# Kernel optimization log

Hardware: AMD Instinct MI355X
Metric: run time of the kernel (lower is better)

Reference implementation:

```python
import jax, jax.numpy as jnp
import numpy as np

ITEM_NUM = 1_000_000
MAXLEN = 200
H = 128
NH = 2
NB = 2
B = 2048
FLOAT_MIN = -1000.0
EPS = 1e-8


def _ln(x, g, b):
    mu = jnp.mean(x, axis=-1, keepdims=True)
    var = jnp.mean((x - mu) ** 2, axis=-1, keepdims=True)
    return (x - mu) / jnp.sqrt(var + EPS) * g + b


def setup_inputs() -> dict:
    key = jax.random.key(0)
    ks = jax.random.split(key, 32)
    s = 1.0 / np.sqrt(H)
    d = {}
    d['user_ids'] = jax.random.randint(ks[0], (B,), 0, 100000)
    d['log_seqs'] = jax.random.randint(ks[1], (B, MAXLEN), 0, ITEM_NUM)
    d['pos_seqs'] = jax.random.randint(ks[2], (B, MAXLEN), 0, ITEM_NUM)
    d['neg_seqs'] = jax.random.randint(ks[3], (B, MAXLEN), 0, ITEM_NUM)
    item = jax.random.normal(ks[4], (ITEM_NUM + 1, H), jnp.float32) * 0.02
    d['item_table'] = item.at[0].set(0.0)  # padding_idx=0
    pos = jax.random.normal(ks[5], (MAXLEN + 1, H), jnp.float32) * 0.02
    d['pos_table'] = pos.at[0].set(0.0)
    # per-block stacked params, torch Linear layout [out,in]
    d['qw'] = jax.random.normal(ks[6], (NB, H, H), jnp.float32) * s
    d['kw'] = jax.random.normal(ks[7], (NB, H, H), jnp.float32) * s
    d['vw'] = jax.random.normal(ks[8], (NB, H, H), jnp.float32) * s
    d['ow'] = jax.random.normal(ks[9], (NB, H, H), jnp.float32) * s
    d['qb'] = jnp.zeros((NB, H), jnp.float32)
    d['kb'] = jnp.zeros((NB, H), jnp.float32)
    d['vb'] = jnp.zeros((NB, H), jnp.float32)
    d['ob'] = jnp.zeros((NB, H), jnp.float32)
    d['w1'] = jax.random.normal(ks[10], (NB, H, H), jnp.float32) * s  # conv1 k=1 == linear
    d['b1'] = jnp.zeros((NB, H), jnp.float32)
    d['w2'] = jax.random.normal(ks[11], (NB, H, H), jnp.float32) * s
    d['b2'] = jnp.zeros((NB, H), jnp.float32)
    d['ln1_g'] = jnp.ones((NB, H), jnp.float32)
    d['ln1_b'] = jnp.zeros((NB, H), jnp.float32)
    d['ln2_g'] = jnp.ones((NB, H), jnp.float32)
    d['ln2_b'] = jnp.zeros((NB, H), jnp.float32)
    d['lnf_g'] = jnp.ones((H,), jnp.float32)
    d['lnf_b'] = jnp.zeros((H,), jnp.float32)
    return d


def reference(item_table, pos_table, qw, qb, kw, kb, vw, vb, ow, ob,
              ln1_g, ln1_b, w1, b1, w2, b2, ln2_g, ln2_b, lnf_g, lnf_b,
              user_ids, log_seqs, pos_seqs, neg_seqs):
    Bb, L = log_seqs.shape
    hd = H // NH
    seqs = item_table[log_seqs] * jnp.asarray(np.sqrt(H), jnp.float32)  # [B,L,H]
    poss = jnp.arange(1, L + 1)[None, :] * (log_seqs != 0)
    seqs = seqs + pos_table[poss]
    causal = jnp.triu(jnp.ones((L, L), bool), k=1)  # True = masked (future)
    for i in range(NB):
        x = seqs
        Q = (x @ qw[i].T + qb[i]).reshape(Bb, L, NH, hd).transpose(0, 2, 1, 3)
        K = (x @ kw[i].T + kb[i]).reshape(Bb, L, NH, hd).transpose(0, 2, 1, 3)
        V = (x @ vw[i].T + vb[i]).reshape(Bb, L, NH, hd).transpose(0, 2, 1, 3)
        scores = jnp.einsum('bhqd,bhkd->bhqk', Q, K) / jnp.asarray(np.sqrt(hd), jnp.float32)
        scores = jnp.where(causal, FLOAT_MIN, scores)
        attn_w = jax.nn.softmax(scores, axis=-1)
        attn = jnp.einsum('bhqk,bhkd->bhqd', attn_w, V)
        attn = attn.transpose(0, 2, 1, 3).reshape(Bb, L, H)
        mha = attn @ ow[i].T + ob[i]
        seqs = _ln(x + mha, ln1_g[i], ln1_b[i])
        ff = jax.nn.relu(seqs @ w1[i].T + b1[i]) @ w2[i].T + b2[i]
        seqs = _ln(seqs + ff, ln2_g[i], ln2_b[i])
    log_feats = _ln(seqs, lnf_g, lnf_b)
    pos_logits = jnp.sum(log_feats * item_table[pos_seqs], axis=-1)
    neg_logits = jnp.sum(log_feats * item_table[neg_seqs], axis=-1)
    return (pos_logits, neg_logits)
```

## Files before the change

### kernel.cpp

```cpp
#include <hip/hip_runtime.h>
#include <math.h>

#define L 200
#define H 128
#define HD 64
#define NB 2
#define BTOT 2048
#define HH (H * H)
#define MTOT (BTOT * L)
#define XSS 136

typedef short bf16x8 __attribute__((ext_vector_type(8)));
typedef float f32x4 __attribute__((ext_vector_type(4)));
typedef unsigned short u16;

#define MFMA16 __builtin_amdgcn_mfma_f32_16x16x32_bf16

__device__ __forceinline__ u16 f2bf(float f) {
    unsigned u = __builtin_bit_cast(unsigned, f);
    u = u + 0x7fffu + ((u >> 16) & 1u);
    return (u16)(u >> 16);
}
__device__ __forceinline__ float bf2f(u16 s) {
    return __builtin_bit_cast(float, ((unsigned)s) << 16);
}
__device__ __forceinline__ bf16x8 pack8(float4 a, float4 b, float sc) {
    bf16x8 r;
    r[0] = (short)f2bf(a.x * sc); r[1] = (short)f2bf(a.y * sc);
    r[2] = (short)f2bf(a.z * sc); r[3] = (short)f2bf(a.w * sc);
    r[4] = (short)f2bf(b.x * sc); r[5] = (short)f2bf(b.y * sc);
    r[6] = (short)f2bf(b.z * sc); r[7] = (short)f2bf(b.w * sc);
    return r;
}

__global__ __launch_bounds__(256) void cvt_kernel(const float* __restrict__ src,
                                                  u16* __restrict__ dst, int n8) {
    int i = blockIdx.x * 256 + threadIdx.x;
    if (i >= n8) return;
    float4 a0 = ((const float4*)src)[i * 2];
    float4 a1 = ((const float4*)src)[i * 2 + 1];
    ((bf16x8*)dst)[i] = pack8(a0, a1, 1.0f);
}

__global__ __launch_bounds__(256) void embed_kernel(const int* __restrict__ ids,
                                                    const float4* __restrict__ item,
                                                    const float4* __restrict__ post,
                                                    u16* __restrict__ X, int M) {
    int idx = blockIdx.x * 256 + threadIdx.x;
    if (idx >= M * 16) return;
    int r = idx >> 4, c8 = idx & 15;
    int id = ids[r];
    int l = r % L;
    int p = (id != 0) ? (l + 1) : 0;
    float4 a0 = item[(size_t)id * 32 + c8 * 2];
    float4 a1 = item[(size_t)id * 32 + c8 * 2 + 1];
    float4 p0 = post[(size_t)p * 32 + c8 * 2];
    float4 p1 = post[(size_t)p * 32 + c8 * 2 + 1];
    const float sc = 11.313708498984761f;
    float4 o0 = make_float4(a0.x * sc + p0.x, a0.y * sc + p0.y, a0.z * sc + p0.z, a0.w * sc + p0.w);
    float4 o1 = make_float4(a1.x * sc + p1.x, a1.y * sc + p1.y, a1.z * sc + p1.z, a1.w * sc + p1.w);
    *(bf16x8*)&X[(size_t)r * 128 + c8 * 8] = pack8(o0, o1, 1.0f);
}

__global__ __launch_bounds__(256) void qkv_kernel(const u16* __restrict__ X,
        const u16* __restrict__ wq, const u16* __restrict__ wk, const u16* __restrict__ wv,
        const float* __restrict__ qb, const float* __restrict__ kb, const float* __restrict__ vb,
        u16* __restrict__ Qo, u16* __restrict__ Ko, u16* __restrict__ Vo, int M) {
    __shared__ u16 Xs[128 * XSS];
    __shared__ u16 Ot[4][16 * XSS];
    int tid = threadIdx.x, w = tid >> 6, lane = tid & 63, g = lane >> 4, l15 = lane & 15;
    int row0 = blockIdx.x * 128;
#pragma unroll
    for (int it = 0; it < 8; ++it) {
        int idx = it * 256 + tid;
        int r = idx >> 4, c8 = idx & 15;
        size_t gr = (size_t)min(row0 + r, M - 1);
        *(bf16x8*)&Xs[r * XSS + c8 * 8] = *(const bf16x8*)(X + gr * 128 + c8 * 8);
    }
    __syncthreads();

    int arow = w * 32 + l15;
    int ko = g * 8;

#pragma unroll
    for (int p = 0; p < 3; ++p) {
        const u16* Wp = p == 0 ? wq : (p == 1 ? wk : wv);
        const float* bp = p == 0 ? qb : (p == 1 ? kb : vb);
        u16* Op = p == 0 ? Qo : (p == 1 ? Ko : Vo);
        const float scale = p == 0 ? 0.125f : 1.0f;

        f32x4 acc[2][8];
#pragma unroll
        for (int nt = 0; nt < 8; ++nt) {
            float bv = bp[nt * 16 + l15];
            acc[0][nt] = (f32x4){bv, bv, bv, bv};
            acc[1][nt] = (f32x4){bv, bv, bv, bv};
        }
#pragma unroll
        for (int kc = 0; kc < 4; ++kc) {
            bf16x8 a0 = *(const bf16x8*)&Xs[arow * XSS + kc * 32 + ko];
            bf16x8 a1 = *(const bf16x8*)&Xs[(arow + 16) * XSS + kc * 32 + ko];
#pragma unroll
            for (int nt = 0; nt < 8; ++nt) {
                bf16x8 b = *(const bf16x8*)(Wp + ((size_t)(nt * 16 + l15) << 7) + kc * 32 + ko);
                acc[0][nt] = MFMA16(a0, b, acc[0][nt], 0, 0, 0);
                acc[1][nt] = MFMA16(a1, b, acc[1][nt], 0, 0, 0);
            }
        }
#pragma unroll
        for (int mt = 0; mt < 2; ++mt) {
#pragma unroll
            for (int r = 0; r < 4; ++r) {
                int ml = g * 4 + r;
#pragma unroll
                for (int nt = 0; nt < 8; ++nt)
                    Ot[w][ml * XSS + nt * 16 + l15] = f2bf(acc[mt][nt][r] * scale);
            }
            asm volatile("s_waitcnt lgkmcnt(0)" ::: "memory");
#pragma unroll
            for (int j = 0; j < 4; ++j) {
                int chunk = j * 64 + lane;
                int rr = chunk >> 4, c16 = chunk & 15;
                bf16x8 v = *(const bf16x8*)&Ot[w][rr * XSS + c16 * 8];
                int grow = row0 + w * 32 + mt * 16 + rr;
                if (grow < M) *(bf16x8*)(Op + (size_t)grow * 128 + c16 * 8) = v;
            }
            asm volatile("s_waitcnt lgkmcnt(0)" ::: "memory");
        }
    }
}

__global__ __launch_bounds__(256) void oproj_ffn1_kernel(const u16* __restrict__ A,
        const u16* __restrict__ Wo, const float* __restrict__ ob,
        const u16* __restrict__ Xres, const float* __restrict__ gma, const float* __restrict__ bta,
        const u16* __restrict__ W1, const float* __restrict__ b1f,
        u16* __restrict__ Xout, u16* __restrict__ F1, int M) {
    __shared__ u16 Xs[128 * XSS];
    __shared__ u16 Ot[4][16 * XSS];
    int tid = threadIdx.x, w = tid >> 6, lane = tid & 63, g = lane >> 4, l15 = lane & 15;
    int row0 = blockIdx.x * 128;
    int rw = row0 + w * 32;
    size_t ar0 = (size_t)min(rw + l15, M - 1) * 128;
    size_t ar1 = (size_t)min(rw + 16 + l15, M - 1) * 128;
    int ko = g * 8;

    f32x4 acc[2][8];
#pragma unroll
    for (int nt = 0; nt < 8; ++nt) {
        float bv = ob[nt * 16 + l15];
        acc[0][nt] = (f32x4){bv, bv, bv, bv};
        acc[1][nt] = (f32x4){bv, bv, bv, bv};
    }
#pragma unroll
    for (int kc = 0; kc < 4; ++kc) {
        bf16x8 a0 = *(const bf16x8*)(A + ar0 + kc * 32 + ko);
        bf16x8 a1 = *(const bf16x8*)(A + ar1 + kc * 32 + ko);
#pragma unroll
        for (int nt = 0; nt < 8; ++nt) {
            bf16x8 b = *(const bf16x8*)(Wo + ((size_t)(nt * 16 + l15) << 7) + kc * 32 + ko);
            acc[0][nt] = MFMA16(a0, b, acc[0][nt], 0, 0, 0);
            acc[1][nt] = MFMA16(a1, b, acc[1][nt], 0, 0, 0);
        }
    }
    float gg[8], bb[8];
#pragma unroll
    for (int nt = 0; nt < 8; ++nt) { gg[nt] = gma[nt * 16 + l15]; bb[nt] = bta[nt * 16 + l15]; }
#pragma unroll
    for (int mt = 0; mt < 2; ++mt) {
#pragma unroll
        for (int r = 0; r < 4; ++r) {
            int rowl = w * 32 + mt * 16 + g * 4 + r;
            size_t rb = (size_t)min(row0 + rowl, M - 1) * 128;
            float v[8];
            float s = 0.f;
#pragma unroll
            for (int nt = 0; nt < 8; ++nt) { v[nt] = acc[mt][nt][r] + bf2f(Xres[rb + nt * 16 + l15]); s += v[nt]; }
            s += __shfl_xor(s, 1); s += __shfl_xor(s, 2); s += __shfl_xor(s, 4); s += __shfl_xor(s, 8);
            float mean = s * 0.0078125f;
            float s2 = 0.f;
#pragma unroll
            for (int nt = 0; nt < 8; ++nt) { float d = v[nt] - mean; s2 += d * d; }
            s2 += __shfl_xor(s2, 1); s2 += __shfl_xor(s2, 2); s2 += __shfl_xor(s2, 4); s2 += __shfl_xor(s2, 8);
            float inv = rsqrtf(s2 * 0.0078125f + 1e-8f);
#pragma unroll
            for (int nt = 0; nt < 8; ++nt)
                Xs[rowl * XSS + nt * 16 + l15] = f2bf((v[nt] - mean) * inv * gg[nt] + bb[nt]);
        }
    }
    __syncthreads();

#pragma unroll
    for (int it = 0; it < 8; ++it) {
        int idx = it * 256 + tid;
        int r = idx >> 4, c8 = idx & 15;
        int grow = row0 + r;
        if (grow < M)
            *(bf16x8*)(Xout + (size_t)grow * 128 + c8 * 8) = *(const bf16x8*)&Xs[r * XSS + c8 * 8];
    }

    int arow = w * 32 + l15;
    f32x4 acc2[2][8];
#pragma unroll
    for (int nt = 0; nt < 8; ++nt) {
        float bv = b1f[nt * 16 + l15];
        acc2[0][nt] = (f32x4){bv, bv, bv, bv};
        acc2[1][nt] = (f32x4){bv, bv, bv, bv};
    }
#pragma unroll
    for (int kc = 0; kc < 4; ++kc) {
        bf16x8 a0 = *(const bf16x8*)&Xs[arow * XSS + kc * 32 + ko];
        bf16x8 a1 = *(const bf16x8*)&Xs[(arow + 16) * XSS + kc * 32 + ko];
#pragma unroll
        for (int nt = 0; nt < 8; ++nt) {
            bf16x8 b = *(const bf16x8*)(W1 + ((size_t)(nt * 16 + l15) << 7) + kc * 32 + ko);
            acc2[0][nt] = MFMA16(a0, b, acc2[0][nt], 0, 0, 0);
            acc2[1][nt] = MFMA16(a1, b, acc2[1][nt], 0, 0, 0);
        }
    }
#pragma unroll
    for (int mt = 0; mt < 2; ++mt) {
#pragma unroll
        for (int r = 0; r < 4; ++r) {
            int ml = g * 4 + r;
#pragma unroll
            for (int nt = 0; nt < 8; ++nt)
                Ot[w][ml * XSS + nt * 16 + l15] = f2bf(fmaxf(acc2[mt][nt][r], 0.f));
        }
        asm volatile("s_waitcnt lgkmcnt(0)" ::: "memory");
#pragma unroll
        for (int j = 0; j < 4; ++j) {
            int chunk = j * 64 + lane;
            int rr = chunk >> 4, c16 = chunk & 15;
            bf16x8 v = *(const bf16x8*)&Ot[w][rr * XSS + c16 * 8];
            int grow = row0 + w * 32 + mt * 16 + rr;
            if (grow < M) *(bf16x8*)(F1 + (size_t)grow * 128 + c16 * 8) = v;
        }
        asm volatile("s_waitcnt lgkmcnt(0)" ::: "memory");
    }
}

__global__ __launch_bounds__(256) void ffn2_ln_kernel(const u16* __restrict__ A,
        const u16* __restrict__ W2, const float* __restrict__ bias,
        const u16* __restrict__ Xres, const float* __restrict__ gma, const float* __restrict__ bta,
        const float* __restrict__ gf, const float* __restrict__ bff, int fin,
        u16* __restrict__ Xout, const float* __restrict__ item,
        const int* __restrict__ pid, const int* __restrict__ nid,
        float* __restrict__ out, int gofs, int M) {
    __shared__ u16 Ot[4][16 * XSS];
    int tid = threadIdx.x, w = tid >> 6, lane = tid & 63, g = lane >> 4, l15 = lane & 15;
    int row0 = blockIdx.x * 128;
    int rw = row0 + w * 32;
    size_t ar0 = (size_t)min(rw + l15, M - 1) * 128;
    size_t ar1 = (size_t)min(rw + 16 + l15, M - 1) * 128;
    int ko = g * 8;

    f32x4 acc[2][8];
#pragma unroll
    for (int nt = 0; nt < 8; ++nt) {
        float bv = bias[nt * 16 + l15];
        acc[0][nt] = (f32x4){bv, bv, bv, bv};
        acc[1][nt] = (f32x4){bv, bv, bv, bv};
    }
#pragma unroll
    for (int kc = 0; kc < 4; ++kc) {
        bf16x8 a0 = *(const bf16x8*)(A + ar0 + kc * 32 + ko);
        bf16x8 a1 = *(const bf16x8*)(A + ar1 + kc * 32 + ko);
#pragma unroll
        for (int nt = 0; nt < 8; ++nt) {
            bf16x8 b = *(const bf16x8*)(W2 + ((size_t)(nt * 16 + l15) << 7) + kc * 32 + ko);
            acc[0][nt] = MFMA16(a0, b, acc[0][nt], 0, 0, 0);
            acc[1][nt] = MFMA16(a1, b, acc[1][nt], 0, 0, 0);
        }
    }
    float gg[8], bb[8], gg2[8], bb2[8];
#pragma unroll
    for (int nt = 0; nt < 8; ++nt) {
        gg[nt] = gma[nt * 16 + l15]; bb[nt] = bta[nt * 16 + l15];
        gg2[nt] = gf[nt * 16 + l15]; bb2[nt] = bff[nt * 16 + l15];
    }
#pragma unroll
    for (int mt = 0; mt < 2; ++mt) {
#pragma unroll
        for (int r = 0; r < 4; ++r) {
            int row = row0 + w * 32 + mt * 16 + g * 4 + r;
            size_t rb = (size_t)min(row, M - 1) * 128;
            float v[8];
            float s = 0.f;
#pragma unroll
            for (int nt = 0; nt < 8; ++nt) { v[nt] = acc[mt][nt][r] + bf2f(Xres[rb + nt * 16 + l15]); s += v[nt]; }
            s += __shfl_xor(s, 1); s += __shfl_xor(s, 2); s += __shfl_xor(s, 4); s += __shfl_xor(s, 8);
            float mean = s * 0.0078125f;
            float s2 = 0.f;
#pragma unroll
            for (int nt = 0; nt < 8; ++nt) { float d = v[nt] - mean; s2 += d * d; }
            s2 += __shfl_xor(s2, 1); s2 += __shfl_xor(s2, 2); s2 += __shfl_xor(s2, 4); s2 += __shfl_xor(s2, 8);
            float inv = rsqrtf(s2 * 0.0078125f + 1e-8f);
#pragma unroll
            for (int nt = 0; nt < 8; ++nt) v[nt] = (v[nt] - mean) * inv * gg[nt] + bb[nt];
            if (fin) {
                float t = 0.f;
#pragma unroll
                for (int nt = 0; nt < 8; ++nt) t += v[nt];
                t += __shfl_xor(t, 1); t += __shfl_xor(t, 2); t += __shfl_xor(t, 4); t += __shfl_xor(t, 8);
                float mean2 = t * 0.0078125f;
                float t2 = 0.f;
#pragma unroll
                for (int nt = 0; nt < 8; ++nt) { float d = v[nt] - mean2; t2 += d * d; }
                t2 += __shfl_xor(t2, 1); t2 += __shfl_xor(t2, 2); t2 += __shfl_xor(t2, 4); t2 += __shfl_xor(t2, 8);
                float inv2 = rsqrtf(t2 * 0.0078125f + 1e-8f);
#pragma unroll
                for (int nt = 0; nt < 8; ++nt) v[nt] = (v[nt] - mean2) * inv2 * gg2[nt] + bb2[nt];
                int gr = gofs + row;
                const float* prow = item + (size_t)pid[gr] * 128;
                const float* nrow = item + (size_t)nid[gr] * 128;
                float sp = 0.f, sn = 0.f;
#pragma unroll
                for (int nt = 0; nt < 8; ++nt) {
                    sp += v[nt] * prow[nt * 16 + l15];
                    sn += v[nt] * nrow[nt * 16 + l15];
                }
                sp += __shfl_xor(sp, 1); sp += __shfl_xor(sp, 2); sp += __shfl_xor(sp, 4); sp += __shfl_xor(sp, 8);
                sn += __shfl_xor(sn, 1); sn += __shfl_xor(sn, 2); sn += __shfl_xor(sn, 4); sn += __shfl_xor(sn, 8);
                if (l15 == 0 && row < M) {
                    out[gr] = sp;
                    out[(size_t)BTOT * L + gr] = sn;
                }
            } else {
                int ml = g * 4 + r;
#pragma unroll
                for (int nt = 0; nt < 8; ++nt)
                    Ot[w][ml * XSS + nt * 16 + l15] = f2bf(v[nt]);
            }
        }
        if (!fin) {
            asm volatile("s_waitcnt lgkmcnt(0)" ::: "memory");
#pragma unroll
            for (int j = 0; j < 4; ++j) {
                int chunk = j * 64 + lane;
                int rr = chunk >> 4, c16 = chunk & 15;
                bf16x8 v = *(const bf16x8*)&Ot[w][rr * XSS + c16 * 8];
                int grow = row0 + w * 32 + mt * 16 + rr;
                if (grow < M) *(bf16x8*)(Xout + (size_t)grow * 128 + c16 * 8) = v;
            }
            asm volatile("s_waitcnt lgkmcnt(0)" ::: "memory");
        }
    }
}

__global__ __launch_bounds__(256, 2) void attn_mfma_kernel(u16* __restrict__ Q,
                                                           const u16* __restrict__ K,
                                                           const u16* __restrict__ V) {
    __shared__ u16 lds_s[64 * 264];
    int b = blockIdx.x >> 1;
    int h = blockIdx.x & 1;
    int tid = threadIdx.x;
    int w = tid >> 6;
    int lane = tid & 63;
    int g = lane >> 4;
    int l15 = lane & 15;

    const u16* Kb = K + ((size_t)b * L) * H + h * HD;
    const u16* Vb = V + ((size_t)b * L) * H + h * HD;
    u16* Qb = Q + ((size_t)b * L) * H + h * HD;

    {
        int d = tid & 63;
        int kq = tid >> 6;
#pragma unroll 8
        for (int it = 0; it < 64; ++it) {
            int k = it * 4 + kq;
            lds_s[d * 264 + k] = Vb[(size_t)min(k, L - 1) * H + d];
        }
    }

    bf16x8 qf[4][2];
    int qrow[4];
#pragma unroll
    for (int nt = 0; nt < 4; ++nt) {
        int q = nt * 64 + w * 16 + l15;
        qrow[nt] = q;
        const u16* src = Qb + (size_t)min(q, L - 1) * H;
        qf[nt][0] = *(const bf16x8*)(src + g * 8);
        qf[nt][1] = *(const bf16x8*)(src + 32 + g * 8);
    }
    __syncthreads();

    f32x4 o[4][4];
    float mrun[4], lrun[4];
#pragma unroll
    for (int i = 0; i < 4; ++i) {
        mrun[i] = -1e30f; lrun[i] = 0.f;
#pragma unroll
        for (int j = 0; j < 4; ++j) o[i][j] = (f32x4){0.f, 0.f, 0.f, 0.f};
    }

    int rp = 8 * (l15 >> 2) + (l15 & 3);
    const f32x4 czero = {0.f, 0.f, 0.f, 0.f};

#pragma unroll
    for (int kc = 0; kc < 4; ++kc) {
        int kbase = kc * 64;
        bf16x8 ka[4][2];
#pragma unroll
        for (int mt = 0; mt < 4; ++mt) {
            int krow = kbase + (mt >> 1) * 32 + (mt & 1) * 4 + rp;
            const u16* src = Kb + (size_t)min(krow, L - 1) * H;
            ka[mt][0] = *(const bf16x8*)(src + g * 8);
            ka[mt][1] = *(const bf16x8*)(src + 32 + g * 8);
        }
#pragma unroll
        for (int nt = 0; nt < 4; ++nt) {
            if (nt < kc) continue;
            int q = qrow[nt];
            f32x4 c[4];
#pragma unroll
            for (int mt = 0; mt < 4; ++mt) {
                c[mt] = MFMA16(ka[mt][0], qf[nt][0], czero, 0, 0, 0);
                c[mt] = MFMA16(ka[mt][1], qf[nt][1], c[mt], 0, 0, 0);
            }
            float pm = -1e30f;
#pragma unroll
            for (int mt = 0; mt < 4; ++mt) {
#pragma unroll
                for (int r = 0; r < 4; ++r) {
                    int kact = kbase + 32 * (mt >> 1) + 4 * (mt & 1) + 8 * g + r;
                    float s = (kact <= q) ? c[mt][r] : -1e30f;
                    c[mt][r] = s;
                    pm = fmaxf(pm, s);
                }
            }
            pm = fmaxf(pm, __shfl_xor(pm, 16));
            pm = fmaxf(pm, __shfl_xor(pm, 32));
            float mnew = fmaxf(mrun[nt], pm);
            float sf = __expf(mrun[nt] - mnew);
            mrun[nt] = mnew;
            float ps = 0.f;
#pragma unroll
            for (int mt = 0; mt < 4; ++mt) {
#pragma unroll
                for (int r = 0; r < 4; ++r) {
                    float p = __expf(c[mt][r] - mnew);
                    c[mt][r] = p;
                    ps += p;
                }
            }
            ps += __shfl_xor(ps, 16);
            ps += __shfl_xor(ps, 32);
            lrun[nt] = lrun[nt] * sf + ps;
#pragma unroll
            for (int md = 0; md < 4; ++md) {
#pragma unroll
                for (int r = 0; r < 4; ++r) o[md][nt][r] *= sf;
            }
#pragma unroll
            for (int ks = 0; ks < 2; ++ks) {
                bf16x8 pb;
#pragma unroll
                for (int j = 0; j < 8; ++j)
                    pb[j] = (short)f2bf(c[2 * ks + (j >> 2)][j & 3]);
#pragma unroll
                for (int md = 0; md < 4; ++md) {
                    const u16* vp = &lds_s[(md * 16 + l15) * 264 + kbase + ks * 32 + g * 8];
                    bf16x8 va = *(const bf16x8*)vp;
                    o[md][nt] = MFMA16(va, pb, o[md][nt], 0, 0, 0);
                }
            }
        }
    }

    __syncthreads();
    u16* Ot = lds_s;
#pragma unroll
    for (int nt = 0; nt < 4; ++nt) {
        float inv = 1.0f / lrun[nt];
        int q = qrow[nt];
        int sw = (q & 7) << 3;
#pragma unroll
        for (int md = 0; md < 4; ++md) {
            int d0 = md * 16 + g * 4;
            unsigned p0 = (unsigned)f2bf(o[md][nt][0] * inv) | ((unsigned)f2bf(o[md][nt][1] * inv) << 16);
            unsigned p1 = (unsigned)f2bf(o[md][nt][2] * inv) | ((unsigned)f2bf(o[md][nt][3] * inv) << 16);
            uint2 u; u.x = p0; u.y = p1;
            *(uint2*)&Ot[q * 64 + (d0 ^ sw)] = u;
        }
    }
    __syncthreads();
    {
        int d = tid & 63;
        for (int q = tid >> 6; q < L; q += 4)
            Qb[(size_t)q * H + d] = Ot[q * 64 + (d ^ ((q & 7) << 3))];
    }
}

extern "C" void kernel_launch(void* const* d_in, const int* in_sizes, int n_in,
                              void* d_out, int out_size, void* d_ws, size_t ws_size,
                              hipStream_t stream) {
    const int* log_seqs = (const int*)d_in[1];
    const int* pos_seqs = (const int*)d_in[2];
    const int* neg_seqs = (const int*)d_in[3];
    const float* item = (const float*)d_in[4];
    const float* post = (const float*)d_in[5];
    const float* qw = (const float*)d_in[6];
    const float* kw = (const float*)d_in[7];
    const float* vw = (const float*)d_in[8];
    const float* ow = (const float*)d_in[9];
    const float* qb = (const float*)d_in[10];
    const float* kb = (const float*)d_in[11];
    const float* vb = (const float*)d_in[12];
    const float* ob = (const float*)d_in[13];
    const float* w1 = (const float*)d_in[14];
    const float* b1 = (const float*)d_in[15];
    const float* w2 = (const float*)d_in[16];
    const float* b2 = (const float*)d_in[17];
    const float* ln1g = (const float*)d_in[18];
    const float* ln1b = (const float*)d_in[19];
    const float* ln2g = (const float*)d_in[20];
    const float* ln2b = (const float*)d_in[21];
    const float* lnfg = (const float*)d_in[22];
    const float* lnfb = (const float*)d_in[23];
    float* out = (float*)d_out;

    int cb = BTOT;
    while (cb > 8 && (size_t)cb * L * H * 8 + 12 * HH * 2 > ws_size) cb >>= 1;
    size_t nbe = (size_t)cb * L * H;
    u16* X16 = (u16*)d_ws;
    u16* Q16 = X16 + nbe;
    u16* K16 = Q16 + nbe;
    u16* V16 = K16 + nbe;
    u16* w16 = V16 + nbe;

    const float* wsrc[6] = {qw, kw, vw, ow, w1, w2};
    int n8 = NB * HH / 8;
    for (int t = 0; t < 6; ++t)
        cvt_kernel<<<(n8 + 255) / 256, 256, 0, stream>>>(wsrc[t], w16 + (size_t)t * NB * HH, n8);

    for (int b0 = 0; b0 < BTOT; b0 += cb) {
        int M = cb * L;
        int gblk = (M + 127) / 128;
        embed_kernel<<<(M * 16 + 255) / 256, 256, 0, stream>>>(log_seqs + (size_t)b0 * L,
                                                               (const float4*)item, (const float4*)post,
                                                               X16, M);
        for (int i = 0; i < NB; ++i) {
            size_t wo = (size_t)i * HH;
            int bofs = i * H;
            qkv_kernel<<<gblk, 256, 0, stream>>>(X16,
                    w16 + 0 * NB * HH + wo, w16 + 1 * NB * HH + wo, w16 + 2 * NB * HH + wo,
                    qb + bofs, kb + bofs, vb + bofs, Q16, K16, V16, M);
            attn_mfma_kernel<<<cb * 2, 256, 0, stream>>>(Q16, K16, V16);
            oproj_ffn1_kernel<<<gblk, 256, 0, stream>>>(Q16, w16 + 3 * NB * HH + wo, ob + bofs,
                    X16, ln1g + bofs, ln1b + bofs,
                    w16 + 4 * NB * HH + wo, b1 + bofs, X16, K16, M);
            ffn2_ln_kernel<<<gblk, 256, 0, stream>>>(K16, w16 + 5 * NB * HH + wo, b2 + bofs,
                    X16, ln2g + bofs, ln2b + bofs, lnfg, lnfb, (i == NB - 1) ? 1 : 0,
                    X16, item, pos_seqs, neg_seqs, out, b0 * L, M);
        }
    }
}
```

Baseline: 1.368 ms.

## Restructure attention loop to iterate query tiles outer, cutting register state

```diff
diff --git a/kernel.cpp b/kernel.cpp
--- a/kernel.cpp
+++ b/kernel.cpp
@@ -372,51 +372,33 @@
             lds_s[d * 264 + k] = Vb[(size_t)min(k, L - 1) * H + d];
         }
     }
-
-    bf16x8 qf[4][2];
-    int qrow[4];
-#pragma unroll
+    __syncthreads();
+
+    int rp = 8 * (l15 >> 2) + (l15 & 3);
+    const f32x4 czero = {0.f, 0.f, 0.f, 0.f};
+
     for (int nt = 0; nt < 4; ++nt) {
         int q = nt * 64 + w * 16 + l15;
-        qrow[nt] = q;
-        const u16* src = Qb + (size_t)min(q, L - 1) * H;
-        qf[nt][0] = *(const bf16x8*)(src + g * 8);
-        qf[nt][1] = *(const bf16x8*)(src + 32 + g * 8);
-    }
-    __syncthreads();
-
-    f32x4 o[4][4];
-    float mrun[4], lrun[4];
-#pragma unroll
-    for (int i = 0; i < 4; ++i) {
-        mrun[i] = -1e30f; lrun[i] = 0.f;
-#pragma unroll
-        for (int j = 0; j < 4; ++j) o[i][j] = (f32x4){0.f, 0.f, 0.f, 0.f};
-    }
-
-    int rp = 8 * (l15 >> 2) + (l15 & 3);
-    const f32x4 czero = {0.f, 0.f, 0.f, 0.f};
-
-#pragma unroll
-    for (int kc = 0; kc < 4; ++kc) {
-        int kbase = kc * 64;
-        bf16x8 ka[4][2];
-#pragma unroll
-        for (int mt = 0; mt < 4; ++mt) {
-            int krow = kbase + (mt >> 1) * 32 + (mt & 1) * 4 + rp;
-            const u16* src = Kb + (size_t)min(krow, L - 1) * H;
-            ka[mt][0] = *(const bf16x8*)(src + g * 8);
-            ka[mt][1] = *(const bf16x8*)(src + 32 + g * 8);
-        }
-#pragma unroll
-        for (int nt = 0; nt < 4; ++nt) {
-            if (nt < kc) continue;
-            int q = qrow[nt];
+        const u16* qsrc = Qb + (size_t)min(q, L - 1) * H;
+        bf16x8 qf0 = *(const bf16x8*)(qsrc + g * 8);
+        bf16x8 qf1 = *(const bf16x8*)(qsrc + 32 + g * 8);
+
+        f32x4 o[4];
+#pragma unroll
+        for (int md = 0; md < 4; ++md) o[md] = czero;
+        float mr = -1e30f, lr = 0.f;
+
+        for (int kc = 0; kc <= nt; ++kc) {
+            int kbase = kc * 64;
             f32x4 c[4];
 #pragma unroll
             for (int mt = 0; mt < 4; ++mt) {
-                c[mt] = MFMA16(ka[mt][0], qf[nt][0], czero, 0, 0, 0);
-                c[mt] = MFMA16(ka[mt][1], qf[nt][1], c[mt], 0, 0, 0);
+                int krow = kbase + (mt >> 1) * 32 + (mt & 1) * 4 + rp;
+                const u16* src = Kb + (size_t)min(krow, L - 1) * H;
+                bf16x8 ka0 = *(const bf16x8*)(src + g * 8);
+                bf16x8 ka1 = *(const bf16x8*)(src + 32 + g * 8);
+                c[mt] = MFMA16(ka0, qf0, czero, 0, 0, 0);
+                c[mt] = MFMA16(ka1, qf1, c[mt], 0, 0, 0);
             }
             float pm = -1e30f;
 #pragma unroll
@@ -431,9 +413,9 @@
             }
             pm = fmaxf(pm, __shfl_xor(pm, 16));
             pm = fmaxf(pm, __shfl_xor(pm, 32));
-            float mnew = fmaxf(mrun[nt], pm);
-            float sf = __expf(mrun[nt] - mnew);
-            mrun[nt] = mnew;
+            float mnew = fmaxf(mr, pm);
+            float sf = __expf(mr - mnew);
+            mr = mnew;
             float ps = 0.f;
 #pragma unroll
             for (int mt = 0; mt < 4; ++mt) {
@@ -446,11 +428,11 @@
             }
             ps += __shfl_xor(ps, 16);
             ps += __shfl_xor(ps, 32);
-            lrun[nt] = lrun[nt] * sf + ps;
+            lr = lr * sf + ps;
 #pragma unroll
             for (int md = 0; md < 4; ++md) {
 #pragma unroll
-                for (int r = 0; r < 4; ++r) o[md][nt][r] *= sf;
+                for (int r = 0; r < 4; ++r) o[md][r] *= sf;
             }
 #pragma unroll
             for (int ks = 0; ks < 2; ++ks) {
@@ -462,33 +444,20 @@
                 for (int md = 0; md < 4; ++md) {
                     const u16* vp = &lds_s[(md * 16 + l15) * 264 + kbase + ks * 32 + g * 8];
                     bf16x8 va = *(const bf16x8*)vp;
-                    o[md][nt] = MFMA16(va, pb, o[md][nt], 0, 0, 0);
+                    o[md] = MFMA16(va, pb, o[md], 0, 0, 0);
                 }
             }
         }
-    }
-
-    __syncthreads();
-    u16* Ot = lds_s;
-#pragma unroll
-    for (int nt = 0; nt < 4; ++nt) {
-        float inv = 1.0f / lrun[nt];
-        int q = qrow[nt];
-        int sw = (q & 7) << 3;
-#pragma unroll
-        for (int md = 0; md < 4; ++md) {
-            int d0 = md * 16 + g * 4;
-            unsigned p0 = (unsigned)f2bf(o[md][nt][0] * inv) | ((unsigned)f2bf(o[md][nt][1] * inv) << 16);
-            unsigned p1 = (unsigned)f2bf(o[md][nt][2] * inv) | ((unsigned)f2bf(o[md][nt][3] * inv) << 16);
-            uint2 u; u.x = p0; u.y = p1;
-            *(uint2*)&Ot[q * 64 + (d0 ^ sw)] = u;
-        }
-    }
-    __syncthreads();
-    {
-        int d = tid & 63;
-        for (int q = tid >> 6; q < L; q += 4)
-            Qb[(size_t)q * H + d] = Ot[q * 64 + (d ^ ((q & 7) << 3))];
+        if (q < L) {
+            float inv = 1.0f / lr;
+#pragma unroll
+            for (int md = 0; md < 4; ++md) {
+                unsigned p0 = (unsigned)f2bf(o[md][0] * inv) | ((unsigned)f2bf(o[md][1] * inv) << 16);
+                unsigned p1 = (unsigned)f2bf(o[md][2] * inv) | ((unsigned)f2bf(o[md][3] * inv) << 16);
+                uint2 uu; uu.x = p0; uu.y = p1;
+                *(uint2*)(Qb + (size_t)q * H + md * 16 + g * 4) = uu;
+            }
+        }
     }
 }
 
```

New measurement: 1.451 ms. 6.0% more time.
